# Performance work log

Hardware: AMD Instinct MI355X
Metric: run time of the kernel (lower is better)

Reference implementation:

```python
import jax, jax.numpy as jnp
import numpy as np

C = 16          # number of classes
LAM = 25.0      # lambda_param (invariance)
MU = 25.0       # mu_param (variance)
NU = 1.0        # nu_param (covariance)
ALPHA = 50.0    # alpha_param (class-discriminative margin & weight)
EPS = 1e-4


def setup_inputs() -> dict:
    key = jax.random.key(0)
    k1, k2, k3 = jax.random.split(key, 3)
    N, D = 32768, 256
    z_a = jax.random.normal(k1, (N, D), dtype=jnp.float32)
    z_b = jax.random.normal(k2, (N, D), dtype=jnp.float32)
    labels = jax.random.randint(k3, (N,), 0, C)
    return {"z_a": z_a, "z_b": z_b, "labels": labels}


def _class_stats(x, labels):
    # counts [C], mean [C,D], unbiased var [C,D] via one segmented pass
    ones = jnp.ones(x.shape[0], x.dtype)
    counts = jax.ops.segment_sum(ones, labels, num_segments=C)
    s = jax.ops.segment_sum(x, labels, num_segments=C)
    sq = jax.ops.segment_sum(x * x, labels, num_segments=C)
    mean = s / counts[:, None]
    var = (sq - counts[:, None] * mean * mean) / (counts[:, None] - 1.0)
    return counts, mean, var


def _variance_loss(var):
    # mean over classes of mean_D relu(1 - std); D equal per class -> global mean
    std = jnp.sqrt(var + EPS)
    return jnp.mean(jax.nn.relu(1.0 - std))


def _covariance_loss(x, labels, counts, mean):
    D = x.shape[1]
    e = x - mean[labels]  # centered per class

    def per_class(c):
        w = (labels == c).astype(x.dtype)
        em = e * w[:, None]
        cov = em.T @ em / (counts[c] - 1.0)  # [D, D]
        off = (cov * cov).sum() - (jnp.diagonal(cov) ** 2).sum()
        return off / D

    return jnp.mean(jax.lax.map(per_class, jnp.arange(C)))


def _class_disc_loss(mean_a, mean_b):
    m = 0.5 * (mean_a + mean_b)               # [C, D]
    diff = m[:, None, :] - m[None, :, :]      # [C, C, D]
    d2 = jnp.sum(diff * diff, axis=-1)        # [C, C]
    mask = jnp.triu(jnp.ones((C, C), bool), 1)
    dist = jnp.sqrt(jnp.where(mask, d2, 1.0))  # safe sqrt off-mask
    pen = jnp.where(mask, jax.nn.relu(ALPHA - dist) ** 2, 0.0)
    npairs = C * (C - 1) // 2
    return pen.sum() / npairs


def reference(z_a, z_b, labels):
    inv_loss = jnp.mean((z_a - z_b) ** 2)
    ca, ma, va = _class_stats(z_a, labels)
    cb, mb, vb = _class_stats(z_b, labels)
    var_loss = 0.5 * (_variance_loss(va) + _variance_loss(vb))
    cov_loss = 0.5 * (_covariance_loss(z_a, labels, ca, ma)
                      + _covariance_loss(z_b, labels, cb, mb))
    class_loss = _class_disc_loss(ma, mb)
    return LAM * inv_loss + MU * var_loss + NU * cov_loss + ALPHA * class_loss
```

## Files before the change

kernel.cpp:

```cpp
#include <hip/hip_runtime.h>
#include <math.h>

#define N_ROWS 32768
#define D 256
#define C 16

#define WS_SUMS_A 0
#define WS_SQ_A   4096
#define WS_SUMS_B 8192
#define WS_SQ_B   12288
#define WS_INV    16384
#define WS_COV    16385
#define WS_COUNTS 16392
#define WS_CURSOR 16408
#define WS_POFFP  16424
#define WS_EOFF   16448
#define WS_INVP   16512
#define WS_COVP   17024
#define WS_PERM   17920
#define WS_ZERO_FLOATS 16408

#define WS_PSUM   50688
#define WS_GPART  181760
#define GP_TILE   16384
#define GP_PER_SPLIT (3 * C * 2 * GP_TILE)
#define NSPLIT    8
#define KC        8
#define RIDX_CAP  1024
#define NEED_A ((size_t)(WS_GPART + NSPLIT * GP_PER_SPLIT) * 4)

typedef __attribute__((ext_vector_type(8))) __bf16 bf16x8;
typedef __attribute__((ext_vector_type(16))) float f32x16;

__device__ inline unsigned bf16_rne(float f) {
    unsigned u = __float_as_uint(f);
    return (u + 0x7fffu + ((u >> 16) & 1u)) >> 16;
}
__device__ inline unsigned pack_bf16(float lo, float hi) {
    return bf16_rne(lo) | (bf16_rne(hi) << 16);
}
__device__ inline int img_base4(int c, int kd) {
    return c * 20 + ((kd + ((c >> 1) & 12)) & 12);
}
__device__ inline int img_base2(int c, int kd) {
    return c * 20 + ((kd + ((c >> 1) & 12)) & 14);
}

__global__ __launch_bounds__(512) void k_hist(const int* __restrict__ labels,
                                              int* __restrict__ counts) {
    __shared__ int h[C];
    const int t = threadIdx.x;
    if (t < C) h[t] = 0;
    __syncthreads();
    const int i = blockIdx.x * 512 + t;
    atomicAdd(&h[labels[i]], 1);
    __syncthreads();
    if (t < C) atomicAdd(&counts[t], h[t]);
}

__global__ void k_scan(const int* __restrict__ counts, int* __restrict__ cursor,
                       int* __restrict__ poffp, int* __restrict__ eoffp) {
    if (threadIdx.x == 0) {
        int off = 0, po = 0;
        for (int c = 0; c < C; ++c) {
            cursor[c] = off;
            eoffp[c] = off;
            poffp[c] = po;
            off += counts[c];
            po += (counts[c] + 31) >> 5;
        }
        poffp[C] = po;
        eoffp[C] = off;
    }
}

__global__ __launch_bounds__(512) void k_scatter(const int* __restrict__ labels,
                                                 int* __restrict__ cursor,
                                                 int* __restrict__ perm) {
    __shared__ int lh[C];
    __shared__ int lbase[C];
    const int t = threadIdx.x;
    if (t < C) lh[t] = 0;
    __syncthreads();
    const int i = blockIdx.x * 512 + t;
    const int lab = labels[i];
    const int lr = atomicAdd(&lh[lab], 1);
    __syncthreads();
    if (t < C) lbase[t] = atomicAdd(&cursor[t], lh[t]);
    __syncthreads();
    perm[lbase[lab] + lr] = i;
}

__global__ __launch_bounds__(256) void k_inv(const float* __restrict__ za,
                                             const float* __restrict__ zb,
                                             float* __restrict__ ws) {
    const int t = threadIdx.x;
    const int base = blockIdx.x * 4096 + t;
    float acc = 0.f;
    #pragma unroll
    for (int k = 0; k < 16; ++k) {
        const int i = base + k * 256;
        const float4 a = ((const float4*)za)[i];
        const float4 b = ((const float4*)zb)[i];
        const float dx = a.x - b.x, dy = a.y - b.y;
        const float dz = a.z - b.z, dw = a.w - b.w;
        acc += dx * dx + dy * dy + dz * dz + dw * dw;
    }
    for (int o = 32; o > 0; o >>= 1) acc += __shfl_down(acc, o, 64);
    __shared__ float red[4];
    if ((t & 63) == 0) red[t >> 6] = acc;
    __syncthreads();
    if (t == 0) ws[WS_INVP + blockIdx.x] = red[0] + red[1] + red[2] + red[3];
}

__global__ __launch_bounds__(256) void k_gram5(const float* __restrict__ za,
                                               const float* __restrict__ zb,
                                               const int* __restrict__ perm,
                                               const int* __restrict__ counts,
                                               const int* __restrict__ poffp,
                                               const int* __restrict__ eoffp,
                                               float* __restrict__ ws) {
    const int t = threadIdx.x;
    const int tile = blockIdx.x >> 3;
    const int split = blockIdx.x & 7;
    const int tx = tile >> 1, ty = (tile + 1) >> 1;
    const int cls = blockIdx.y, inp = blockIdx.z;
    const float* X = inp ? zb : za;
    const int cnt = counts[cls];
    const int eoff = eoffp[cls];
    const int nsteps = poffp[cls + 1] - poffp[cls];
    const int chunk = (nsteps + NSPLIT - 1) / NSPLIT;
    const int sb = split * chunk;
    const int se = min(sb + chunk, nsteps);
    const bool diag = (tx == ty);
    const int cm0 = tx * 128, cn0 = ty * 128;

    __shared__ __align__(16) unsigned img[2][2][2560];
    __shared__ float sstats[512];
    __shared__ int ridx[RIDX_CAP];

    for (int i = t; i < 512; i += 256) sstats[i] = 0.f;
    const int nl = (se > sb) ? (se - sb) * 32 : 0;
    for (int i = t; i < min(nl, RIDX_CAP); i += 256) {
        const int gr = sb * 32 + i;
        ridx[i] = (gr < cnt) ? perm[eoff + gr] : -1;
    }
    __syncthreads();

    auto rowidx = [&](int li) -> int {
        if (li < RIDX_CAP) return ridx[li];
        const int gr = sb * 32 + li;
        return (gr < cnt) ? perm[eoff + gr] : -1;
    };

    const int lane = t & 63, w = t >> 6;
    const int wr = w & 1, wc = w >> 1;
    const int cg = lane & 31, q = lane >> 5;

    int img_sel, lc, kp0, nIt;
    if (diag) {
        img_sel = 0; lc = 4 * (t & 31); kp0 = 2 * (t >> 5); nIt = 2;
    } else {
        const int half = t >> 7, u = t & 127;
        img_sel = half; lc = 4 * (u & 31); kp0 = 4 * (u >> 5); nIt = 4;
    }
    const int gcol = (diag ? cm0 : (img_sel ? cn0 : cm0)) + lc;

    f32x16 acc[2][2];
    #pragma unroll
    for (int i = 0; i < 2; ++i)
        #pragma unroll
        for (int j = 0; j < 2; ++j) acc[i][j] = 0.0f;

    float s1r[4] = {0.f, 0.f, 0.f, 0.f};
    float s2r[4] = {0.f, 0.f, 0.f, 0.f};
    float4 f0[4], f1[4];

    auto load_regs = [&](int s) {
        #pragma unroll
        for (int it = 0; it < 4; ++it) if (it < nIt) {
            const int li = (s - sb) * 32 + 2 * (kp0 + it);
            const int r0 = rowidx(li), r1 = rowidx(li + 1);
            f0[it] = (r0 >= 0) ? *(const float4*)(X + (size_t)r0 * D + gcol)
                               : make_float4(0.f, 0.f, 0.f, 0.f);
            f1[it] = (r1 >= 0) ? *(const float4*)(X + (size_t)r1 * D + gcol)
                               : make_float4(0.f, 0.f, 0.f, 0.f);
        }
    };
    auto pack_store = [&](int buf) {
        if (!diag) {
            unsigned pwq[4][4];
            #pragma unroll
            for (int it = 0; it < 4; ++it) {
                pwq[0][it] = pack_bf16(f0[it].x, f1[it].x);
                pwq[1][it] = pack_bf16(f0[it].y, f1[it].y);
                pwq[2][it] = pack_bf16(f0[it].z, f1[it].z);
                pwq[3][it] = pack_bf16(f0[it].w, f1[it].w);
            }
            #pragma unroll
            for (int d = 0; d < 4; ++d)
                *(uint4*)&img[buf][img_sel][img_base4(lc + d, kp0)] =
                    make_uint4(pwq[d][0], pwq[d][1], pwq[d][2], pwq[d][3]);
            if (tile == 1) {
                #pragma unroll
                for (int it = 0; it < 4; ++it) {
                    s1r[0] += f0[it].x + f1[it].x; s2r[0] += f0[it].x * f0[it].x + f1[it].x * f1[it].x;
                    s1r[1] += f0[it].y + f1[it].y; s2r[1] += f0[it].y * f0[it].y + f1[it].y * f1[it].y;
                    s1r[2] += f0[it].z + f1[it].z; s2r[2] += f0[it].z * f0[it].z + f1[it].z * f1[it].z;
                    s1r[3] += f0[it].w + f1[it].w; s2r[3] += f0[it].w * f0[it].w + f1[it].w * f1[it].w;
                }
            }
        } else {
            unsigned pwq[4][2];
            #pragma unroll
            for (int it = 0; it < 2; ++it) {
                pwq[0][it] = pack_bf16(f0[it].x, f1[it].x);
                pwq[1][it] = pack_bf16(f0[it].y, f1[it].y);
                pwq[2][it] = pack_bf16(f0[it].z, f1[it].z);
                pwq[3][it] = pack_bf16(f0[it].w, f1[it].w);
            }
            #pragma unroll
            for (int d = 0; d < 4; ++d)
                *(uint2*)&img[buf][0][img_base2(lc + d, kp0)] =
                    make_uint2(pwq[d][0], pwq[d][1]);
        }
    };
    auto frag = [&](int buf, int sel, int col, int kd) -> bf16x8 {
        return *(const bf16x8*)&img[buf][sel][img_base4(col, kd)];
    };

    const int bch = diag ? 0 : 1;
    if (sb < se) {
        load_regs(sb);
        pack_store(0);
        __syncthreads();
        for (int s = sb; s < se; ++s) {
            const int buf = (s - sb) & 1;
            const bool more = (s + 1 < se);
            if (more) load_regs(s + 1);
            #pragma unroll
            for (int h = 0; h < 2; ++h) {
                bf16x8 a[2], b[2];
                #pragma unroll
                for (int i = 0; i < 2; ++i) {
                    a[i] = frag(buf, 0,   wr * 64 + i * 32 + cg, h * 8 + q * 4);
                    b[i] = frag(buf, bch, wc * 64 + i * 32 + cg, h * 8 + q * 4);
                }
                acc[0][0] = __builtin_amdgcn_mfma_f32_32x32x16_bf16(a[0], b[0], acc[0][0], 0, 0, 0);
                acc[0][1] = __builtin_amdgcn_mfma_f32_32x32x16_bf16(a[0], b[1], acc[0][1], 0, 0, 0);
                acc[1][0] = __builtin_amdgcn_mfma_f32_32x32x16_bf16(a[1], b[0], acc[1][0], 0, 0, 0);
                acc[1][1] = __builtin_amdgcn_mfma_f32_32x32x16_bf16(a[1], b[1], acc[1][1], 0, 0, 0);
            }
            if (more) pack_store(buf ^ 1);
            __syncthreads();
        }
    }

    float* gp = ws + WS_GPART + (size_t)split * GP_PER_SPLIT
              + ((size_t)tile * C * 2 + cls * 2 + inp) * GP_TILE;
    #pragma unroll
    for (int i = 0; i < 2; ++i)
        #pragma unroll
        for (int j = 0; j < 2; ++j)
            #pragma unroll
            for (int r = 0; r < 16; ++r) {
                const int row = wr * 64 + i * 32 + (r & 3) + 8 * (r >> 2) + 4 * q;
                const int col = wc * 64 + j * 32 + cg;
                gp[row * 128 + col] = acc[i][j][r];
            }

    if (tile == 1) {
        const int c0 = img_sel * 128 + lc;
        #pragma unroll
        for (int d = 0; d < 4; ++d) {
            atomicAdd(&sstats[c0 + d],       s1r[d]);
            atomicAdd(&sstats[256 + c0 + d], s2r[d]);
        }
        __syncthreads();
        const size_t base = (((size_t)split * C + cls) * 2 + inp) * 512;
        ws[WS_PSUM + base + t]       = sstats[t];
        ws[WS_PSUM + base + 256 + t] = sstats[256 + t];
    }
}

__global__ __launch_bounds__(256) void k_reduce2(float* __restrict__ ws) {
    const int t = threadIdx.x;
    const int c = blockIdx.x;
    const int stat = blockIdx.y & 1, inp = blockIdx.y >> 1;
    float acc = 0.f;
    #pragma unroll
    for (int sp = 0; sp < NSPLIT; ++sp)
        acc += ws[WS_PSUM + (((size_t)sp * C + c) * 2 + inp) * 512 + stat * 256 + t];
    const int base = stat ? (inp ? WS_SQ_B : WS_SQ_A)
                          : (inp ? WS_SUMS_B : WS_SUMS_A);
    ws[base + c * D + t] = acc;
}

__global__ __launch_bounds__(256) void k_cov(const int* __restrict__ counts,
                                             float* __restrict__ ws) {
    const int t = threadIdx.x;
    const int tile = blockIdx.x / KC, k0 = blockIdx.x % KC;
    const int tx = tile >> 1, ty = (tile + 1) >> 1;
    const int cls = blockIdx.y, inp = blockIdx.z;
    const int cnt = counts[cls];
    const float fc = (float)cnt;
    const float cinv = 1.f / fc, uinv = 1.f / (fc - 1.f);
    const float wgt = (tx == ty) ? 1.f : 2.f;
    const int cm0 = tx * 128, cn0 = ty * 128;
    __shared__ float M[D];
    const float* sums = ws + (inp ? WS_SUMS_B : WS_SUMS_A) + cls * D;
    M[t] = sums[t] * cinv;
    __syncthreads();

    const float* gp0 = ws + WS_GPART + ((size_t)tile * C * 2 + cls * 2 + inp) * GP_TILE;
    float local = 0.f;
    #pragma unroll
    for (int kk = 0; kk < 64 / KC; ++kk) {
        const int e = (k0 * (64 / KC) + kk) * 256 + t;
        float g = 0.f;
        #pragma unroll
        for (int s = 0; s < NSPLIT; ++s)
            g += gp0[(size_t)s * GP_PER_SPLIT + e];
        const int row = e >> 7, col = e & 127;
        const int gm = cm0 + row, gn = cn0 + col;
        const float cov = (g - fc * M[gm] * M[gn]) * uinv;
        if (gm != gn) local += wgt * cov * cov;
    }
    for (int o = 32; o > 0; o >>= 1) local += __shfl_down(local, o, 64);
    __shared__ float red[4];
    if ((t & 63) == 0) red[t >> 6] = local;
    __syncthreads();
    if (t == 0)
        ws[WS_COVP + (((size_t)inp * C + cls) * 3 + tile) * KC + k0] =
            red[0] + red[1] + red[2] + red[3];
}

__global__ __launch_bounds__(256) void k_stats(const float* __restrict__ za,
                                               const float* __restrict__ zb,
                                               const int* __restrict__ labels,
                                               float* __restrict__ ws) {
    const int t = threadIdx.x;
    __shared__ float S[4][C * D];
    __shared__ int lab[512];
    for (int i = t; i < 4 * C * D; i += 256) ((float*)S)[i] = 0.f;
    const int r0 = blockIdx.x * 512;
    for (int i = t; i < 512; i += 256) lab[i] = labels[r0 + i];
    __syncthreads();
    float invp = 0.f;
    #pragma unroll 4
    for (int rr = 0; rr < 512; ++rr) {
        const int l = lab[rr];
        const float a = za[(size_t)(r0 + rr) * D + t];
        const float b = zb[(size_t)(r0 + rr) * D + t];
        const float dd = a - b;
        invp += dd * dd;
        S[0][l * D + t] += a;
        S[1][l * D + t] += a * a;
        S[2][l * D + t] += b;
        S[3][l * D + t] += b * b;
    }
    __syncthreads();
    #pragma unroll
    for (int c = 0; c < C; ++c) {
        atomicAdd(&ws[WS_SUMS_A + c * D + t], S[0][c * D + t]);
        atomicAdd(&ws[WS_SQ_A   + c * D + t], S[1][c * D + t]);
        atomicAdd(&ws[WS_SUMS_B + c * D + t], S[2][c * D + t]);
        atomicAdd(&ws[WS_SQ_B   + c * D + t], S[3][c * D + t]);
    }
    for (int o = 32; o > 0; o >>= 1) invp += __shfl_down(invp, o, 64);
    if ((t & 63) == 0) atomicAdd(&ws[WS_INV], invp);
}

#define STR 20
#define KB 32
__global__ __launch_bounds__(256) void k_gram_slow(const float* __restrict__ za,
                                                   const float* __restrict__ zb,
                                                   const int* __restrict__ perm,
                                                   const int* __restrict__ counts,
                                                   float* __restrict__ ws) {
    const int t = threadIdx.x;
    const int tile = blockIdx.x;
    const int tx = tile >> 1, ty = (tile + 1) >> 1;
    const int cls = blockIdx.y;
    const int inp = blockIdx.z;
    const float* X = inp ? zb : za;
    const float* sums = ws + (inp ? WS_SUMS_B : WS_SUMS_A) + cls * D;
    int offs = 0;
    for (int c = 0; c < cls; ++c) offs += counts[c];
    const int cnt = counts[cls];
    const int cm0 = tx * 128, cn0 = ty * 128;
    __shared__ __align__(16) unsigned lds[2][256 * STR];
    const int p = t >> 5, cq = t & 31;
    const int lane = t & 63, w = t >> 6;
    const int wr = w & 1, wc = w >> 1;
    const int cg = lane & 31, q = lane >> 5;
    f32x16 acc[2][2];
    #pragma unroll
    for (int i = 0; i < 2; ++i)
        #pragma unroll
        for (int j = 0; j < 2; ++j) acc[i][j] = 0.0f;
    const int nsteps = (cnt + KB - 1) / KB;
    auto stage = [&](int buf, int k0) {
        #pragma unroll
        for (int ch = 0; ch < 2; ++ch) {
            const int gc = (ch ? cn0 : cm0) + 4 * cq;
            #pragma unroll
            for (int sub = 0; sub < 2; ++sub) {
                const int rr = sub * 16 + 2 * p;
                const int r0 = k0 + rr, r1 = r0 + 1;
                float4 v0 = make_float4(0.f, 0.f, 0.f, 0.f), v1 = v0;
                if (r0 < cnt) v0 = *(const float4*)(X + (size_t)perm[offs + r0] * D + gc);
                if (r1 < cnt) v1 = *(const float4*)(X + (size_t)perm[offs + r1] * D + gc);
                unsigned* dst = &lds[buf][(ch * 128 + 4 * cq) * STR + (rr >> 1)];
                dst[0 * STR] = pack_bf16(v0.x, v1.x);
                dst[1 * STR] = pack_bf16(v0.y, v1.y);
                dst[2 * STR] = pack_bf16(v0.z, v1.z);
                dst[3 * STR] = pack_bf16(v0.w, v1.w);
            }
        }
    };
    auto frag = [&](int buf, int colbase, int h) -> bf16x8 {
        return *(const bf16x8*)&lds[buf][(colbase + cg) * STR + h * 8 + q * 4];
    };
    stage(0, 0);
    for (int s = 0; s < nsteps; ++s) {
        __syncthreads();
        const int buf = s & 1;
        if (s + 1 < nsteps) stage(buf ^ 1, (s + 1) * KB);
        #pragma unroll
        for (int h = 0; h < 2; ++h) {
            bf16x8 a0 = frag(buf, wr * 64, h);
            bf16x8 a1 = frag(buf, wr * 64 + 32, h);
            bf16x8 b0 = frag(buf, 128 + wc * 64, h);
            bf16x8 b1 = frag(buf, 128 + wc * 64 + 32, h);
            acc[0][0] = __builtin_amdgcn_mfma_f32_32x32x16_bf16(a0, b0, acc[0][0], 0, 0, 0);
            acc[0][1] = __builtin_amdgcn_mfma_f32_32x32x16_bf16(a0, b1, acc[0][1], 0, 0, 0);
            acc[1][0] = __builtin_amdgcn_mfma_f32_32x32x16_bf16(a1, b0, acc[1][0], 0, 0, 0);
            acc[1][1] = __builtin_amdgcn_mfma_f32_32x32x16_bf16(a1, b1, acc[1][1], 0, 0, 0);
        }
    }
    const float fc = (float)cnt;
    const float cinv = 1.f / fc, uinv = 1.f / (fc - 1.f);
    const float wgt = (tx == ty) ? 1.f : 2.f;
    float local = 0.f;
    #pragma unroll
    for (int i = 0; i < 2; ++i) {
        #pragma unroll
        for (int j = 0; j < 2; ++j) {
            const int gn = cn0 + wc * 64 + j * 32 + (lane & 31);
            const float mn = sums[gn] * cinv;
            #pragma unroll
            for (int r = 0; r < 16; ++r) {
                const int row = (r & 3) + 8 * (r >> 2) + 4 * q;
                const int gm = cm0 + wr * 64 + i * 32 + row;
                const float cov = (acc[i][j][r] - fc * (sums[gm] * cinv) * mn) * uinv;
                if (gm != gn) local += wgt * cov * cov;
            }
        }
    }
    for (int o = 32; o > 0; o >>= 1) local += __shfl_down(local, o, 64);
    if (lane == 0) atomicAdd(&ws[WS_COV], local);
}

__global__ __launch_bounds__(256) void k_final(const float* __restrict__ ws,
                                               float* __restrict__ out,
                                               int fast) {
    __shared__ float M[C * D];
    __shared__ float redv[4], redi[4], redc[4], redp[4];
    const int t = threadIdx.x;
    const int* counts = (const int*)ws + WS_COUNTS;

    float vsum = 0.f;
    for (int idx = t; idx < 2 * C * D; idx += 256) {
        const int inp = idx >> 12;
        const int cd = idx & 4095;
        const int c = cd >> 8;
        const float cnt = (float)counts[c];
        const float s  = ws[(inp ? WS_SUMS_B : WS_SUMS_A) + cd];
        const float sq = ws[(inp ? WS_SQ_B   : WS_SQ_A)   + cd];
        const float mean = s / cnt;
        const float var = (sq - cnt * mean * mean) / (cnt - 1.f);
        vsum += fmaxf(1.f - sqrtf(var + 1e-4f), 0.f);
    }
    float isum, csum;
    if (fast) {
        isum = ws[WS_INVP + t] + ws[WS_INVP + 256 + t];
        csum = ws[WS_COVP + t] + ws[WS_COVP + 256 + t] + ws[WS_COVP + 512 + t];
    } else {
        isum = (t == 0) ? ws[WS_INV] : 0.f;
        csum = (t == 0) ? ws[WS_COV] : 0.f;
    }
    for (int cd = t; cd < C * D; cd += 256) {
        const int c = cd >> 8;
        const float cnt = (float)counts[c];
        M[cd] = 0.5f * (ws[WS_SUMS_A + cd] + ws[WS_SUMS_B + cd]) / cnt;
    }
    for (int o = 32; o > 0; o >>= 1) {
        vsum += __shfl_down(vsum, o, 64);
        isum += __shfl_down(isum, o, 64);
        csum += __shfl_down(csum, o, 64);
    }
    if ((t & 63) == 0) {
        redv[t >> 6] = vsum; redi[t >> 6] = isum; redc[t >> 6] = csum;
    }
    __syncthreads();

    const int wv = t >> 6, ln = t & 63;
    float psum = 0.f;
    int p = 0;
    for (int i = 0; i < C; ++i) {
        for (int j = i + 1; j < C; ++j, ++p) {
            if ((p & 3) != wv) continue;
            float d2 = 0.f;
            #pragma unroll
            for (int d = ln; d < D; d += 64) {
                const float df = M[i * D + d] - M[j * D + d];
                d2 += df * df;
            }
            for (int o = 32; o > 0; o >>= 1) d2 += __shfl_down(d2, o, 64);
            if (ln == 0) {
                const float dist = sqrtf(d2);
                const float r = fmaxf(50.f - dist, 0.f);
                psum += r * r;
            }
        }
    }
    if (ln == 0) redp[wv] = psum;
    __syncthreads();

    if (t == 0) {
        const float var_loss = (redv[0] + redv[1] + redv[2] + redv[3]) / 8192.f;
        const float class_loss = (redp[0] + redp[1] + redp[2] + redp[3]) / 120.f;
        const float inv_loss = (redi[0] + redi[1] + redi[2] + redi[3]) / (float)(N_ROWS * D);
        const float cov_loss = 0.5f * (redc[0] + redc[1] + redc[2] + redc[3]) / (float)(C * D);
        out[0] = 25.f * inv_loss + 25.f * var_loss + 1.f * cov_loss + 50.f * class_loss;
    }
}

extern "C" void kernel_launch(void* const* d_in, const int* in_sizes, int n_in,
                              void* d_out, int out_size, void* d_ws, size_t ws_size,
                              hipStream_t stream) {
    const float* za = (const float*)d_in[0];
    const float* zb = (const float*)d_in[1];
    const int* labels = (const int*)d_in[2];
    float* out = (float*)d_out;
    float* ws = (float*)d_ws;
    int* wsi = (int*)d_ws;

    hipMemsetAsync(d_ws, 0, WS_ZERO_FLOATS * sizeof(float), stream);
    k_hist<<<64, 512, 0, stream>>>(labels, wsi + WS_COUNTS);
    k_scan<<<1, 64, 0, stream>>>(wsi + WS_COUNTS, wsi + WS_CURSOR,
                                 wsi + WS_POFFP, wsi + WS_EOFF);
    k_scatter<<<64, 512, 0, stream>>>(labels, wsi + WS_CURSOR, wsi + WS_PERM);

    if (ws_size >= NEED_A) {
        k_inv<<<512, 256, 0, stream>>>(za, zb, ws);
        k_gram5<<<dim3(3 * NSPLIT, C, 2), 256, 0, stream>>>(
            za, zb, wsi + WS_PERM, wsi + WS_COUNTS, wsi + WS_POFFP,
            wsi + WS_EOFF, ws);
        k_reduce2<<<dim3(C, 4), 256, 0, stream>>>(ws);
        k_cov<<<dim3(3 * KC, C, 2), 256, 0, stream>>>(wsi + WS_COUNTS, ws);
        k_final<<<1, 256, 0, stream>>>(ws, out, 1);
    } else {
        k_stats<<<64, 256, 0, stream>>>(za, zb, labels, ws);
        k_gram_slow<<<dim3(3, C, 2), 256, 0, stream>>>(za, zb, wsi + WS_PERM,
                                                       wsi + WS_COUNTS, ws);
        k_final<<<1, 256, 0, stream>>>(ws, out, 0);
    }
}
```

Measured before the change: 173.0 us.

## Fuse histogram into inv pass, deterministic scatter, one-block-per-class Gram with 64x64 tasks

The label histogram moves into the invariance-loss kernel as per-block partial counts. A new scatter kernel computes prefix offsets from those partials, which removes the memset, the separate hist and scan kernels and the global atomics. The Gram kernel now uses one 640-thread block per (split, class, input) that stages all 256 columns once and computes the 10 upper-triangular 64x64 tiles, one per wave, instead of three separate 128x128 tile blocks that each reload the rows. Covariance reduction is adapted to the new tile layout; the trade-off is fewer blocks and larger shared memory per block.

```diff
diff --git a/kernel.cpp b/kernel.cpp
--- a/kernel.cpp
+++ b/kernel.cpp
@@ -21,13 +21,15 @@
 #define WS_ZERO_FLOATS 16408
 
 #define WS_PSUM   50688
-#define WS_GPART  181760
-#define GP_TILE   16384
-#define GP_PER_SPLIT (3 * C * 2 * GP_TILE)
+#define WS_HPART  181760
+#define WS_GPART2 189952
+#define GP_TILE2  4096
+#define NTASK     10
 #define NSPLIT    8
-#define KC        8
+#define K2        2
+#define GP_PER_SPLIT2 (NTASK * C * 2 * GP_TILE2)
 #define RIDX_CAP  1024
-#define NEED_A ((size_t)(WS_GPART + NSPLIT * GP_PER_SPLIT) * 4)
+#define NEED_A ((size_t)(WS_GPART2 + NSPLIT * GP_PER_SPLIT2) * 4)
 
 typedef __attribute__((ext_vector_type(8))) __bf16 bf16x8;
 typedef __attribute__((ext_vector_type(16))) float f32x16;
@@ -44,6 +46,291 @@
 }
 __device__ inline int img_base2(int c, int kd) {
     return c * 20 + ((kd + ((c >> 1) & 12)) & 14);
+}
+__device__ inline void task_rc(int w, int& r, int& c) {
+    if (w < 4)      { r = 0; c = w; }
+    else if (w < 7) { r = 1; c = w - 3; }
+    else if (w < 9) { r = 2; c = w - 5; }
+    else            { r = 3; c = 3; }
+}
+
+
+__global__ __launch_bounds__(256) void k_pre(const float* __restrict__ za,
+                                             const float* __restrict__ zb,
+                                             const int* __restrict__ labels,
+                                             int* __restrict__ hpart,
+                                             float* __restrict__ ws) {
+    const int t = threadIdx.x;
+    const int b = blockIdx.x;
+    __shared__ int h[C];
+    if (t < C) h[t] = 0;
+    __syncthreads();
+    if (t < 64) atomicAdd(&h[labels[b * 64 + t]], 1);
+
+    const int base = b * 4096 + t;
+    float acc = 0.f;
+    #pragma unroll
+    for (int k = 0; k < 16; ++k) {
+        const int i = base + k * 256;
+        const float4 a = ((const float4*)za)[i];
+        const float4 v = ((const float4*)zb)[i];
+        const float dx = a.x - v.x, dy = a.y - v.y;
+        const float dz = a.z - v.z, dw = a.w - v.w;
+        acc += dx * dx + dy * dy + dz * dz + dw * dw;
+    }
+    for (int o = 32; o > 0; o >>= 1) acc += __shfl_down(acc, o, 64);
+    __shared__ float red[4];
+    if ((t & 63) == 0) red[t >> 6] = acc;
+    __syncthreads();
+    if (t < C) hpart[b * C + t] = h[t];
+    if (t == 0) ws[WS_INVP + b] = red[0] + red[1] + red[2] + red[3];
+}
+
+__global__ __launch_bounds__(512) void k_scatter2(const int* __restrict__ labels,
+                                                  const int* __restrict__ hpart,
+                                                  int* __restrict__ counts,
+                                                  int* __restrict__ poffp,
+                                                  int* __restrict__ eoffp,
+                                                  int* __restrict__ perm) {
+    const int t = threadIdx.x;
+    const int B = blockIdx.x;
+    __shared__ int lh[C];
+    __shared__ int tot[32][C];
+    __shared__ int pre[32][C];
+    __shared__ int ccnt[C], cpre[C], ceoff[C];
+    const int i = B * 512 + t;
+    const int lab = labels[i];
+    if (t < C) lh[t] = 0;
+    const int c = t & 15, seg = t >> 4;
+    {
+        int tt = 0, pp = 0;
+        const int plo = seg * 16, pcut = B * 8;
+        #pragma unroll
+        for (int p = plo; p < plo + 16; ++p) {
+            const int v = hpart[p * C + c];
+            tt += v;
+            if (p < pcut) pp += v;
+        }
+        tot[seg][c] = tt;
+        pre[seg][c] = pp;
+    }
+    __syncthreads();
+    const int lr = atomicAdd(&lh[lab], 1);
+    if (t < C) {
+        int s1 = 0, s2 = 0;
+        #pragma unroll
+        for (int g = 0; g < 32; ++g) { s1 += tot[g][t]; s2 += pre[g][t]; }
+        ccnt[t] = s1;
+        cpre[t] = s2;
+    }
+    __syncthreads();
+    if (t == 0) {
+        int off = 0, po = 0;
+        for (int cc = 0; cc < C; ++cc) {
+            ceoff[cc] = off;
+            if (B == 0) { eoffp[cc] = off; poffp[cc] = po; counts[cc] = ccnt[cc]; }
+            off += ccnt[cc];
+            po += (ccnt[cc] + 31) >> 5;
+        }
+        if (B == 0) { eoffp[C] = off; poffp[C] = po; }
+    }
+    __syncthreads();
+    perm[ceoff[lab] + cpre[lab] + lr] = i;
+}
+
+__global__ __launch_bounds__(640) void k_gram6(const float* __restrict__ za,
+                                               const float* __restrict__ zb,
+                                               const int* __restrict__ perm,
+                                               const int* __restrict__ counts,
+                                               const int* __restrict__ poffp,
+                                               const int* __restrict__ eoffp,
+                                               float* __restrict__ ws) {
+    const int t = threadIdx.x;
+    const int split = blockIdx.x;
+    const int cls = blockIdx.y, inp = blockIdx.z;
+    const float* X = inp ? zb : za;
+    const int cnt = counts[cls];
+    const int eoff = eoffp[cls];
+    const int nsteps = poffp[cls + 1] - poffp[cls];
+    const int chunk = (nsteps + NSPLIT - 1) / NSPLIT;
+    const int sb = split * chunk;
+    const int se = min(sb + chunk, nsteps);
+
+    __shared__ __align__(16) unsigned img[2][5120];
+    __shared__ float sstats[512];
+    __shared__ int ridx[RIDX_CAP];
+
+    for (int i = t; i < 512; i += 640) sstats[i] = 0.f;
+    const int nl = (se > sb) ? (se - sb) * 32 : 0;
+    for (int i = t; i < nl && i < RIDX_CAP; i += 640) {
+        const int gr = sb * 32 + i;
+        ridx[i] = (gr < cnt) ? perm[eoff + gr] : -1;
+    }
+    __syncthreads();
+
+    auto rowidx = [&](int li) -> int {
+        if (li < RIDX_CAP) return ridx[li];
+        const int gr = sb * 32 + li;
+        return (gr < cnt) ? perm[eoff + gr] : -1;
+    };
+
+    const int lane = t & 63, w = t >> 6;
+    const int cg = lane & 31, q = lane >> 5;
+    int tr, tc;
+    task_rc(w, tr, tc);
+    const bool stg = (t < 512);
+
+    const int lc = 4 * (t & 63);
+    const int kp0 = 2 * ((t >> 6) & 7);
+
+    f32x16 acc[2][2];
+    #pragma unroll
+    for (int i = 0; i < 2; ++i)
+        #pragma unroll
+        for (int j = 0; j < 2; ++j) acc[i][j] = 0.0f;
+
+    float s1r[4] = {0.f, 0.f, 0.f, 0.f};
+    float s2r[4] = {0.f, 0.f, 0.f, 0.f};
+    float4 f0[2], f1[2];
+
+    auto load_regs = [&](int s) {
+        #pragma unroll
+        for (int it = 0; it < 2; ++it) {
+            const int li = (s - sb) * 32 + 2 * (kp0 + it);
+            const int r0 = rowidx(li), r1 = rowidx(li + 1);
+            f0[it] = (r0 >= 0) ? *(const float4*)(X + (size_t)r0 * D + lc)
+                               : make_float4(0.f, 0.f, 0.f, 0.f);
+            f1[it] = (r1 >= 0) ? *(const float4*)(X + (size_t)r1 * D + lc)
+                               : make_float4(0.f, 0.f, 0.f, 0.f);
+        }
+    };
+    auto pack_store = [&](int buf) {
+        unsigned pw[4][2];
+        #pragma unroll
+        for (int it = 0; it < 2; ++it) {
+            pw[0][it] = pack_bf16(f0[it].x, f1[it].x);
+            pw[1][it] = pack_bf16(f0[it].y, f1[it].y);
+            pw[2][it] = pack_bf16(f0[it].z, f1[it].z);
+            pw[3][it] = pack_bf16(f0[it].w, f1[it].w);
+        }
+        #pragma unroll
+        for (int d = 0; d < 4; ++d)
+            *(uint2*)&img[buf][img_base2(lc + d, kp0)] = make_uint2(pw[d][0], pw[d][1]);
+        #pragma unroll
+        for (int it = 0; it < 2; ++it) {
+            s1r[0] += f0[it].x + f1[it].x; s2r[0] += f0[it].x * f0[it].x + f1[it].x * f1[it].x;
+            s1r[1] += f0[it].y + f1[it].y; s2r[1] += f0[it].y * f0[it].y + f1[it].y * f1[it].y;
+            s1r[2] += f0[it].z + f1[it].z; s2r[2] += f0[it].z * f0[it].z + f1[it].z * f1[it].z;
+            s1r[3] += f0[it].w + f1[it].w; s2r[3] += f0[it].w * f0[it].w + f1[it].w * f1[it].w;
+        }
+    };
+    auto frag = [&](int buf, int col, int kd) -> bf16x8 {
+        return *(const bf16x8*)&img[buf][img_base4(col, kd)];
+    };
+
+    if (sb < se) {
+        if (stg) { load_regs(sb); pack_store(0); }
+        __syncthreads();
+        for (int s = sb; s < se; ++s) {
+            const int buf = (s - sb) & 1;
+            const bool more = (s + 1 < se);
+            if (stg && more) load_regs(s + 1);
+            #pragma unroll
+            for (int h = 0; h < 2; ++h) {
+                const int kd = h * 8 + q * 4;
+                bf16x8 a0 = frag(buf, tr * 64 + cg, kd);
+                bf16x8 a1 = frag(buf, tr * 64 + 32 + cg, kd);
+                bf16x8 b0, b1;
+                if (tr == tc) { b0 = a0; b1 = a1; }
+                else {
+                    b0 = frag(buf, tc * 64 + cg, kd);
+                    b1 = frag(buf, tc * 64 + 32 + cg, kd);
+                }
+                acc[0][0] = __builtin_amdgcn_mfma_f32_32x32x16_bf16(a0, b0, acc[0][0], 0, 0, 0);
+                acc[0][1] = __builtin_amdgcn_mfma_f32_32x32x16_bf16(a0, b1, acc[0][1], 0, 0, 0);
+                acc[1][0] = __builtin_amdgcn_mfma_f32_32x32x16_bf16(a1, b0, acc[1][0], 0, 0, 0);
+                acc[1][1] = __builtin_amdgcn_mfma_f32_32x32x16_bf16(a1, b1, acc[1][1], 0, 0, 0);
+            }
+            if (stg && more) pack_store(buf ^ 1);
+            __syncthreads();
+        }
+    }
+
+    float* gp = ws + WS_GPART2 + (size_t)split * GP_PER_SPLIT2
+              + (((size_t)cls * 2 + inp) * NTASK + w) * GP_TILE2;
+    #pragma unroll
+    for (int i = 0; i < 2; ++i)
+        #pragma unroll
+        for (int j = 0; j < 2; ++j)
+            #pragma unroll
+            for (int r = 0; r < 16; ++r) {
+                const int row = i * 32 + (r & 3) + 8 * (r >> 2) + 4 * q;
+                const int col = j * 32 + cg;
+                gp[row * 64 + col] = acc[i][j][r];
+            }
+
+    if (stg) {
+        #pragma unroll
+        for (int d = 0; d < 4; ++d) {
+            atomicAdd(&sstats[lc + d],       s1r[d]);
+            atomicAdd(&sstats[256 + lc + d], s2r[d]);
+        }
+    }
+    __syncthreads();
+    const size_t pbase = (((size_t)split * C + cls) * 2 + inp) * 512;
+    for (int i = t; i < 512; i += 640) ws[WS_PSUM + pbase + i] = sstats[i];
+}
+
+__global__ __launch_bounds__(256) void k_reduce2(float* __restrict__ ws) {
+    const int t = threadIdx.x;
+    const int c = blockIdx.x;
+    const int stat = blockIdx.y & 1, inp = blockIdx.y >> 1;
+    float acc = 0.f;
+    #pragma unroll
+    for (int sp = 0; sp < NSPLIT; ++sp)
+        acc += ws[WS_PSUM + (((size_t)sp * C + c) * 2 + inp) * 512 + stat * 256 + t];
+    const int base = stat ? (inp ? WS_SQ_B : WS_SQ_A)
+                          : (inp ? WS_SUMS_B : WS_SUMS_A);
+    ws[base + c * D + t] = acc;
+}
+
+__global__ __launch_bounds__(256) void k_cov2(const int* __restrict__ counts,
+                                              float* __restrict__ ws) {
+    const int t = threadIdx.x;
+    const int w = blockIdx.x / K2, k0 = blockIdx.x % K2;
+    int tr, tc;
+    task_rc(w, tr, tc);
+    const int cls = blockIdx.y, inp = blockIdx.z;
+    const int cnt = counts[cls];
+    const float fc = (float)cnt;
+    const float cinv = 1.f / fc, uinv = 1.f / (fc - 1.f);
+    const float wgt = (tr == tc) ? 1.f : 2.f;
+    __shared__ float Mr[64], Mc[64];
+    const float* sums = ws + (inp ? WS_SUMS_B : WS_SUMS_A) + cls * D;
+    if (t < 64) Mr[t] = sums[tr * 64 + t] * cinv;
+    else if (t < 128) Mc[t - 64] = sums[tc * 64 + (t - 64)] * cinv;
+    __syncthreads();
+
+    const float* gp0 = ws + WS_GPART2 + (((size_t)cls * 2 + inp) * NTASK + w) * GP_TILE2;
+    float local = 0.f;
+    #pragma unroll
+    for (int kk = 0; kk < 2048 / 256; ++kk) {
+        const int e = k0 * 2048 + kk * 256 + t;
+        float g = 0.f;
+        #pragma unroll
+        for (int sp = 0; sp < NSPLIT; ++sp)
+            g += gp0[(size_t)sp * GP_PER_SPLIT2 + e];
+        const int row = e >> 6, col = e & 63;
+        const float cov = (g - fc * Mr[row] * Mc[col]) * uinv;
+        if (!(tr == tc && row == col)) local += wgt * cov * cov;
+    }
+    for (int o = 32; o > 0; o >>= 1) local += __shfl_down(local, o, 64);
+    __shared__ float red[4];
+    if ((t & 63) == 0) red[t >> 6] = local;
+    __syncthreads();
+    if (t == 0)
+        ws[WS_COVP + (((size_t)inp * C + cls) * NTASK + w) * K2 + k0] =
+            red[0] + red[1] + red[2] + red[3];
 }
 
 __global__ __launch_bounds__(512) void k_hist(const int* __restrict__ labels,
@@ -89,250 +376,6 @@
     if (t < C) lbase[t] = atomicAdd(&cursor[t], lh[t]);
     __syncthreads();
     perm[lbase[lab] + lr] = i;
-}
-
-__global__ __launch_bounds__(256) void k_inv(const float* __restrict__ za,
-                                             const float* __restrict__ zb,
-                                             float* __restrict__ ws) {
-    const int t = threadIdx.x;
-    const int base = blockIdx.x * 4096 + t;
-    float acc = 0.f;
-    #pragma unroll
-    for (int k = 0; k < 16; ++k) {
-        const int i = base + k * 256;
-        const float4 a = ((const float4*)za)[i];
-        const float4 b = ((const float4*)zb)[i];
-        const float dx = a.x - b.x, dy = a.y - b.y;
-        const float dz = a.z - b.z, dw = a.w - b.w;
-        acc += dx * dx + dy * dy + dz * dz + dw * dw;
-    }
-    for (int o = 32; o > 0; o >>= 1) acc += __shfl_down(acc, o, 64);
-    __shared__ float red[4];
-    if ((t & 63) == 0) red[t >> 6] = acc;
-    __syncthreads();
-    if (t == 0) ws[WS_INVP + blockIdx.x] = red[0] + red[1] + red[2] + red[3];
-}
-
-__global__ __launch_bounds__(256) void k_gram5(const float* __restrict__ za,
-                                               const float* __restrict__ zb,
-                                               const int* __restrict__ perm,
-                                               const int* __restrict__ counts,
-                                               const int* __restrict__ poffp,
-                                               const int* __restrict__ eoffp,
-                                               float* __restrict__ ws) {
-    const int t = threadIdx.x;
-    const int tile = blockIdx.x >> 3;
-    const int split = blockIdx.x & 7;
-    const int tx = tile >> 1, ty = (tile + 1) >> 1;
-    const int cls = blockIdx.y, inp = blockIdx.z;
-    const float* X = inp ? zb : za;
-    const int cnt = counts[cls];
-    const int eoff = eoffp[cls];
-    const int nsteps = poffp[cls + 1] - poffp[cls];
-    const int chunk = (nsteps + NSPLIT - 1) / NSPLIT;
-    const int sb = split * chunk;
-    const int se = min(sb + chunk, nsteps);
-    const bool diag = (tx == ty);
-    const int cm0 = tx * 128, cn0 = ty * 128;
-
-    __shared__ __align__(16) unsigned img[2][2][2560];
-    __shared__ float sstats[512];
-    __shared__ int ridx[RIDX_CAP];
-
-    for (int i = t; i < 512; i += 256) sstats[i] = 0.f;
-    const int nl = (se > sb) ? (se - sb) * 32 : 0;
-    for (int i = t; i < min(nl, RIDX_CAP); i += 256) {
-        const int gr = sb * 32 + i;
-        ridx[i] = (gr < cnt) ? perm[eoff + gr] : -1;
-    }
-    __syncthreads();
-
-    auto rowidx = [&](int li) -> int {
-        if (li < RIDX_CAP) return ridx[li];
-        const int gr = sb * 32 + li;
-        return (gr < cnt) ? perm[eoff + gr] : -1;
-    };
-
-    const int lane = t & 63, w = t >> 6;
-    const int wr = w & 1, wc = w >> 1;
-    const int cg = lane & 31, q = lane >> 5;
-
-    int img_sel, lc, kp0, nIt;
-    if (diag) {
-        img_sel = 0; lc = 4 * (t & 31); kp0 = 2 * (t >> 5); nIt = 2;
-    } else {
-        const int half = t >> 7, u = t & 127;
-        img_sel = half; lc = 4 * (u & 31); kp0 = 4 * (u >> 5); nIt = 4;
-    }
-    const int gcol = (diag ? cm0 : (img_sel ? cn0 : cm0)) + lc;
-
-    f32x16 acc[2][2];
-    #pragma unroll
-    for (int i = 0; i < 2; ++i)
-        #pragma unroll
-        for (int j = 0; j < 2; ++j) acc[i][j] = 0.0f;
-
-    float s1r[4] = {0.f, 0.f, 0.f, 0.f};
-    float s2r[4] = {0.f, 0.f, 0.f, 0.f};
-    float4 f0[4], f1[4];
-
-    auto load_regs = [&](int s) {
-        #pragma unroll
-        for (int it = 0; it < 4; ++it) if (it < nIt) {
-            const int li = (s - sb) * 32 + 2 * (kp0 + it);
-            const int r0 = rowidx(li), r1 = rowidx(li + 1);
-            f0[it] = (r0 >= 0) ? *(const float4*)(X + (size_t)r0 * D + gcol)
-                               : make_float4(0.f, 0.f, 0.f, 0.f);
-            f1[it] = (r1 >= 0) ? *(const float4*)(X + (size_t)r1 * D + gcol)
-                               : make_float4(0.f, 0.f, 0.f, 0.f);
-        }
-    };
-    auto pack_store = [&](int buf) {
-        if (!diag) {
-            unsigned pwq[4][4];
-            #pragma unroll
-            for (int it = 0; it < 4; ++it) {
-                pwq[0][it] = pack_bf16(f0[it].x, f1[it].x);
-                pwq[1][it] = pack_bf16(f0[it].y, f1[it].y);
-                pwq[2][it] = pack_bf16(f0[it].z, f1[it].z);
-                pwq[3][it] = pack_bf16(f0[it].w, f1[it].w);
-            }
-            #pragma unroll
-            for (int d = 0; d < 4; ++d)
-                *(uint4*)&img[buf][img_sel][img_base4(lc + d, kp0)] =
-                    make_uint4(pwq[d][0], pwq[d][1], pwq[d][2], pwq[d][3]);
-            if (tile == 1) {
-                #pragma unroll
-                for (int it = 0; it < 4; ++it) {
-                    s1r[0] += f0[it].x + f1[it].x; s2r[0] += f0[it].x * f0[it].x + f1[it].x * f1[it].x;
-                    s1r[1] += f0[it].y + f1[it].y; s2r[1] += f0[it].y * f0[it].y + f1[it].y * f1[it].y;
-                    s1r[2] += f0[it].z + f1[it].z; s2r[2] += f0[it].z * f0[it].z + f1[it].z * f1[it].z;
-                    s1r[3] += f0[it].w + f1[it].w; s2r[3] += f0[it].w * f0[it].w + f1[it].w * f1[it].w;
-                }
-            }
-        } else {
-            unsigned pwq[4][2];
-            #pragma unroll
-            for (int it = 0; it < 2; ++it) {
-                pwq[0][it] = pack_bf16(f0[it].x, f1[it].x);
-                pwq[1][it] = pack_bf16(f0[it].y, f1[it].y);
-                pwq[2][it] = pack_bf16(f0[it].z, f1[it].z);
-                pwq[3][it] = pack_bf16(f0[it].w, f1[it].w);
-            }
-            #pragma unroll
-            for (int d = 0; d < 4; ++d)
-                *(uint2*)&img[buf][0][img_base2(lc + d, kp0)] =
-                    make_uint2(pwq[d][0], pwq[d][1]);
-        }
-    };
-    auto frag = [&](int buf, int sel, int col, int kd) -> bf16x8 {
-        return *(const bf16x8*)&img[buf][sel][img_base4(col, kd)];
-    };
-
-    const int bch = diag ? 0 : 1;
-    if (sb < se) {
-        load_regs(sb);
-        pack_store(0);
-        __syncthreads();
-        for (int s = sb; s < se; ++s) {
-            const int buf = (s - sb) & 1;
-            const bool more = (s + 1 < se);
-            if (more) load_regs(s + 1);
-            #pragma unroll
-            for (int h = 0; h < 2; ++h) {
-                bf16x8 a[2], b[2];
-                #pragma unroll
-                for (int i = 0; i < 2; ++i) {
-                    a[i] = frag(buf, 0,   wr * 64 + i * 32 + cg, h * 8 + q * 4);
-                    b[i] = frag(buf, bch, wc * 64 + i * 32 + cg, h * 8 + q * 4);
-                }
-                acc[0][0] = __builtin_amdgcn_mfma_f32_32x32x16_bf16(a[0], b[0], acc[0][0], 0, 0, 0);
-                acc[0][1] = __builtin_amdgcn_mfma_f32_32x32x16_bf16(a[0], b[1], acc[0][1], 0, 0, 0);
-                acc[1][0] = __builtin_amdgcn_mfma_f32_32x32x16_bf16(a[1], b[0], acc[1][0], 0, 0, 0);
-                acc[1][1] = __builtin_amdgcn_mfma_f32_32x32x16_bf16(a[1], b[1], acc[1][1], 0, 0, 0);
-            }
-            if (more) pack_store(buf ^ 1);
-            __syncthreads();
-        }
-    }
-
-    float* gp = ws + WS_GPART + (size_t)split * GP_PER_SPLIT
-              + ((size_t)tile * C * 2 + cls * 2 + inp) * GP_TILE;
-    #pragma unroll
-    for (int i = 0; i < 2; ++i)
-        #pragma unroll
-        for (int j = 0; j < 2; ++j)
-            #pragma unroll
-            for (int r = 0; r < 16; ++r) {
-                const int row = wr * 64 + i * 32 + (r & 3) + 8 * (r >> 2) + 4 * q;
-                const int col = wc * 64 + j * 32 + cg;
-                gp[row * 128 + col] = acc[i][j][r];
-            }
-
-    if (tile == 1) {
-        const int c0 = img_sel * 128 + lc;
-        #pragma unroll
-        for (int d = 0; d < 4; ++d) {
-            atomicAdd(&sstats[c0 + d],       s1r[d]);
-            atomicAdd(&sstats[256 + c0 + d], s2r[d]);
-        }
-        __syncthreads();
-        const size_t base = (((size_t)split * C + cls) * 2 + inp) * 512;
-        ws[WS_PSUM + base + t]       = sstats[t];
-        ws[WS_PSUM + base + 256 + t] = sstats[256 + t];
-    }
-}
-
-__global__ __launch_bounds__(256) void k_reduce2(float* __restrict__ ws) {
-    const int t = threadIdx.x;
-    const int c = blockIdx.x;
-    const int stat = blockIdx.y & 1, inp = blockIdx.y >> 1;
-    float acc = 0.f;
-    #pragma unroll
-    for (int sp = 0; sp < NSPLIT; ++sp)
-        acc += ws[WS_PSUM + (((size_t)sp * C + c) * 2 + inp) * 512 + stat * 256 + t];
-    const int base = stat ? (inp ? WS_SQ_B : WS_SQ_A)
-                          : (inp ? WS_SUMS_B : WS_SUMS_A);
-    ws[base + c * D + t] = acc;
-}
-
-__global__ __launch_bounds__(256) void k_cov(const int* __restrict__ counts,
-                                             float* __restrict__ ws) {
-    const int t = threadIdx.x;
-    const int tile = blockIdx.x / KC, k0 = blockIdx.x % KC;
-    const int tx = tile >> 1, ty = (tile + 1) >> 1;
-    const int cls = blockIdx.y, inp = blockIdx.z;
-    const int cnt = counts[cls];
-    const float fc = (float)cnt;
-    const float cinv = 1.f / fc, uinv = 1.f / (fc - 1.f);
-    const float wgt = (tx == ty) ? 1.f : 2.f;
-    const int cm0 = tx * 128, cn0 = ty * 128;
-    __shared__ float M[D];
-    const float* sums = ws + (inp ? WS_SUMS_B : WS_SUMS_A) + cls * D;
-    M[t] = sums[t] * cinv;
-    __syncthreads();
-
-    const float* gp0 = ws + WS_GPART + ((size_t)tile * C * 2 + cls * 2 + inp) * GP_TILE;
-    float local = 0.f;
-    #pragma unroll
-    for (int kk = 0; kk < 64 / KC; ++kk) {
-        const int e = (k0 * (64 / KC) + kk) * 256 + t;
-        float g = 0.f;
-        #pragma unroll
-        for (int s = 0; s < NSPLIT; ++s)
-            g += gp0[(size_t)s * GP_PER_SPLIT + e];
-        const int row = e >> 7, col = e & 127;
-        const int gm = cm0 + row, gn = cn0 + col;
-        const float cov = (g - fc * M[gm] * M[gn]) * uinv;
-        if (gm != gn) local += wgt * cov * cov;
-    }
-    for (int o = 32; o > 0; o >>= 1) local += __shfl_down(local, o, 64);
-    __shared__ float red[4];
-    if ((t & 63) == 0) red[t >> 6] = local;
-    __syncthreads();
-    if (t == 0)
-        ws[WS_COVP + (((size_t)inp * C + cls) * 3 + tile) * KC + k0] =
-            red[0] + red[1] + red[2] + red[3];
 }
 
 __global__ __launch_bounds__(256) void k_stats(const float* __restrict__ za,
@@ -485,7 +528,8 @@
     float isum, csum;
     if (fast) {
         isum = ws[WS_INVP + t] + ws[WS_INVP + 256 + t];
-        csum = ws[WS_COVP + t] + ws[WS_COVP + 256 + t] + ws[WS_COVP + 512 + t];
+        csum = ws[WS_COVP + t] + ws[WS_COVP + 256 + t]
+             + ((t < 128) ? ws[WS_COVP + 512 + t] : 0.f);
     } else {
         isum = (t == 0) ? ws[WS_INV] : 0.f;
         csum = (t == 0) ? ws[WS_COV] : 0.f;
@@ -547,21 +591,22 @@
     float* ws = (float*)d_ws;
     int* wsi = (int*)d_ws;
 
-    hipMemsetAsync(d_ws, 0, WS_ZERO_FLOATS * sizeof(float), stream);
-    k_hist<<<64, 512, 0, stream>>>(labels, wsi + WS_COUNTS);
-    k_scan<<<1, 64, 0, stream>>>(wsi + WS_COUNTS, wsi + WS_CURSOR,
-                                 wsi + WS_POFFP, wsi + WS_EOFF);
-    k_scatter<<<64, 512, 0, stream>>>(labels, wsi + WS_CURSOR, wsi + WS_PERM);
-
     if (ws_size >= NEED_A) {
-        k_inv<<<512, 256, 0, stream>>>(za, zb, ws);
-        k_gram5<<<dim3(3 * NSPLIT, C, 2), 256, 0, stream>>>(
+        k_pre<<<512, 256, 0, stream>>>(za, zb, labels, wsi + WS_HPART, ws);
+        k_scatter2<<<64, 512, 0, stream>>>(labels, wsi + WS_HPART, wsi + WS_COUNTS,
+                                           wsi + WS_POFFP, wsi + WS_EOFF, wsi + WS_PERM);
+        k_gram6<<<dim3(NSPLIT, C, 2), 640, 0, stream>>>(
             za, zb, wsi + WS_PERM, wsi + WS_COUNTS, wsi + WS_POFFP,
             wsi + WS_EOFF, ws);
         k_reduce2<<<dim3(C, 4), 256, 0, stream>>>(ws);
-        k_cov<<<dim3(3 * KC, C, 2), 256, 0, stream>>>(wsi + WS_COUNTS, ws);
+        k_cov2<<<dim3(NTASK * K2, C, 2), 256, 0, stream>>>(wsi + WS_COUNTS, ws);
         k_final<<<1, 256, 0, stream>>>(ws, out, 1);
     } else {
+        hipMemsetAsync(d_ws, 0, WS_ZERO_FLOATS * sizeof(float), stream);
+        k_hist<<<64, 512, 0, stream>>>(labels, wsi + WS_COUNTS);
+        k_scan<<<1, 64, 0, stream>>>(wsi + WS_COUNTS, wsi + WS_CURSOR,
+                                     wsi + WS_POFFP, wsi + WS_EOFF);
+        k_scatter<<<64, 512, 0, stream>>>(labels, wsi + WS_CURSOR, wsi + WS_PERM);
         k_stats<<<64, 256, 0, stream>>>(za, zb, labels, ws);
         k_gram_slow<<<dim3(3, C, 2), 256, 0, stream>>>(za, zb, wsi + WS_PERM,
                                                        wsi + WS_COUNTS, ws);
```

Result: faster. 161.7 us (-6.6%).
